# Kernel tuning notes

Measured on AMD Instinct MI355X. Metric: run time of the kernel, lower is better.

Reference implementation:

```python
import jax, jax.numpy as jnp
import numpy as np
from jax import lax

TOP_K = 6
NORM_MIN = 1e-12


def setup_inputs() -> dict:
    key = jax.random.key(0)
    k0, k1, k2, k3, k4, k5 = jax.random.split(key, 6)
    B, S, H, E, I = 2, 1024, 2048, 64, 512
    return {
        "hidden_states": jax.random.normal(k0, (B, S, H), dtype=jnp.float32),
        "gate_w": jax.random.normal(k1, (E, H), dtype=jnp.float32) * 0.02,
        "e_bias": jax.random.normal(k2, (E,), dtype=jnp.float32) * 0.01,
        "gate_proj": jax.random.normal(k3, (E, H, I), dtype=jnp.float32) * 0.02,
        "up_proj": jax.random.normal(k4, (E, H, I), dtype=jnp.float32) * 0.02,
        "down_proj": jax.random.normal(k5, (E, I, H), dtype=jnp.float32) * 0.02,
    }


def reference(hidden_states, gate_w, e_bias, gate_proj, up_proj, down_proj):
    B, S, H = hidden_states.shape
    E = gate_w.shape[0]
    x = hidden_states.reshape(-1, H)                      # [T, H]
    T = x.shape[0]

    # --- routing (done in float32 in the original) ---
    router_logits = x.astype(jnp.float32) @ gate_w.T      # [T, E]
    routing_probs = jax.nn.softmax(router_logits, axis=-1)
    # topk over bias-corrected scores, but weights come from raw probs
    _, selected = lax.top_k(routing_probs + e_bias[None, :], TOP_K)  # [T, k]
    w = jnp.take_along_axis(routing_probs, selected, axis=-1)        # [T, k]
    w = w / jnp.clip(w.sum(axis=-1, keepdims=True), NORM_MIN)
    w = w.astype(hidden_states.dtype)

    # combine weights: [T, E], zero for unselected experts
    combine = jnp.zeros((T, E), dtype=hidden_states.dtype)
    combine = combine.at[jnp.arange(T)[:, None], selected].add(w)

    # --- experts: SwiGLU MLP per expert, weighted-sum combine ---
    def step(acc, params):
        wg, wu, wd, c = params                            # wg,wu [H,I]; wd [I,H]; c [T]
        h = jax.nn.silu(x @ wg) * (x @ wu)                # [T, I]
        return acc + (h @ wd) * c[:, None], None

    init = jnp.zeros((T, H), dtype=hidden_states.dtype)
    final, _ = lax.scan(step, init, (gate_proj, up_proj, down_proj, combine.T))
    return final.reshape(-1), router_logits.reshape(-1)
```

## Files before the change

kernel.cpp:

```cpp
#include <hip/hip_runtime.h>
#include <math.h>

#define T_TOK 2048
#define H_DIM 2048
#define E_NUM 64
#define I_DIM 512
#define TOPK  6
#define NPAIR (T_TOK * TOPK)
#define MAXTILES 80

typedef __attribute__((ext_vector_type(8))) short s8;
typedef __attribute__((ext_vector_type(4))) float f4;
typedef __attribute__((ext_vector_type(8))) unsigned short u16x8;

static __device__ __forceinline__ unsigned short f2bf(float f) {
  unsigned int u = __float_as_uint(f);
  u += 0x7fff + ((u >> 16) & 1);
  return (unsigned short)(u >> 16);
}
static __device__ __forceinline__ unsigned int cvt_pk(float lo, float hi) {
  unsigned int r;
  asm("v_cvt_pk_bf16_f32 %0, %1, %2" : "=v"(r) : "v"(lo), "v"(hi));
  return r;
}
static __device__ __forceinline__ void gload_lds16(const void* g, void* l) {
  __builtin_amdgcn_global_load_lds(
      (const __attribute__((address_space(1))) unsigned int*)g,
      (__attribute__((address_space(3))) unsigned int*)l, 16, 0, 0);
}
#define SBAR()      __builtin_amdgcn_s_barrier()
#define SCHED0()    __builtin_amdgcn_sched_barrier(0)
#define WAIT_LGKM0() asm volatile("s_waitcnt lgkmcnt(0)" ::: "memory")
#define WAIT_VM0()   asm volatile("s_waitcnt vmcnt(0)" ::: "memory")
#define WAIT_VM2()   asm volatile("s_waitcnt vmcnt(2)" ::: "memory")
#define WAIT_VM4()   asm volatile("s_waitcnt vmcnt(4)" ::: "memory")

__global__ __launch_bounds__(512) void router_kernel(
    const float* __restrict__ x, const float* __restrict__ gw,
    const float* __restrict__ ebias, float* __restrict__ logits_out,
    int* __restrict__ sel, float* __restrict__ wsel)
{
  __shared__ float xs[4][H_DIM];
  __shared__ float lg[4][E_NUM];
  int t0 = blockIdx.x * 4;
  int tid = threadIdx.x;
  {
    float4* xsv = (float4*)&xs[0][0];
    const float4* src = (const float4*)(x + (size_t)t0 * H_DIM);
    for (int i = tid; i < 4 * H_DIM / 4; i += 512) xsv[i] = src[i];
  }
  __syncthreads();

  int wave = tid >> 6, lane = tid & 63;
  for (int ii = 0; ii < 4; ++ii) {
    int e0 = wave * 8 + ii * 2, e1 = e0 + 1;
    const float4* g0 = (const float4*)(gw + (size_t)e0 * H_DIM);
    const float4* g1 = (const float4*)(gw + (size_t)e1 * H_DIM);
    float s00=0.f,s01=0.f,s02=0.f,s03=0.f, s10=0.f,s11=0.f,s12=0.f,s13=0.f;
    for (int h4 = lane; h4 < H_DIM / 4; h4 += 64) {
      float4 w0 = g0[h4], w1 = g1[h4];
      float4 a0 = ((const float4*)xs[0])[h4];
      float4 a1 = ((const float4*)xs[1])[h4];
      float4 a2 = ((const float4*)xs[2])[h4];
      float4 a3 = ((const float4*)xs[3])[h4];
      s00 += w0.x*a0.x + w0.y*a0.y + w0.z*a0.z + w0.w*a0.w;
      s01 += w0.x*a1.x + w0.y*a1.y + w0.z*a1.z + w0.w*a1.w;
      s02 += w0.x*a2.x + w0.y*a2.y + w0.z*a2.z + w0.w*a2.w;
      s03 += w0.x*a3.x + w0.y*a3.y + w0.z*a3.z + w0.w*a3.w;
      s10 += w1.x*a0.x + w1.y*a0.y + w1.z*a0.z + w1.w*a0.w;
      s11 += w1.x*a1.x + w1.y*a1.y + w1.z*a1.z + w1.w*a1.w;
      s12 += w1.x*a2.x + w1.y*a2.y + w1.z*a2.z + w1.w*a2.w;
      s13 += w1.x*a3.x + w1.y*a3.y + w1.z*a3.z + w1.w*a3.w;
    }
    for (int off = 32; off; off >>= 1) {
      s00 += __shfl_down(s00, off); s01 += __shfl_down(s01, off);
      s02 += __shfl_down(s02, off); s03 += __shfl_down(s03, off);
      s10 += __shfl_down(s10, off); s11 += __shfl_down(s11, off);
      s12 += __shfl_down(s12, off); s13 += __shfl_down(s13, off);
    }
    if (lane == 0) {
      lg[0][e0]=s00; lg[1][e0]=s01; lg[2][e0]=s02; lg[3][e0]=s03;
      lg[0][e1]=s10; lg[1][e1]=s11; lg[2][e1]=s12; lg[3][e1]=s13;
    }
  }
  __syncthreads();

  if (tid < 256) {
    int tt = tid >> 6, e = tid & 63;
    logits_out[(size_t)(t0 + tt) * E_NUM + e] = lg[tt][e];
  }

  if (wave == 0) {
    for (int tt = 0; tt < 4; ++tt) {
      int t = t0 + tt;
      float v = lg[tt][lane];
      float m = v;
      for (int off = 32; off; off >>= 1) m = fmaxf(m, __shfl_xor(m, off));
      float ex = __expf(v - m);
      float sum = ex;
      for (int off = 32; off; off >>= 1) sum += __shfl_xor(sum, off);
      float prob = ex / sum;
      float sc = prob + ebias[lane];

      int selidx[TOPK]; float selw[TOPK]; float wsum = 0.f;
      #pragma unroll
      for (int k = 0; k < TOPK; ++k) {
        float mm = sc;
        for (int off = 32; off; off >>= 1) mm = fmaxf(mm, __shfl_xor(mm, off));
        unsigned long long ball = __ballot(sc == mm);
        int s = __ffsll(ball) - 1;
        float p = __shfl(prob, s);
        selidx[k] = s; selw[k] = p; wsum += p;
        if (lane == s) sc = -INFINITY;
      }
      if (lane == 0) {
        float inv = 1.f / fmaxf(wsum, 1e-12f);
        #pragma unroll
        for (int k = 0; k < TOPK; ++k) {
          sel[t * TOPK + k] = selidx[k];
          wsel[t * TOPK + k] = selw[k] * inv;
        }
      }
    }
  }
}

__global__ __launch_bounds__(64) void build_lists(
    const int* __restrict__ sel, const float* __restrict__ wsel,
    int* __restrict__ cnt, int* __restrict__ toklist, float* __restrict__ wtlist,
    int* __restrict__ posmap)
{
  int e = blockIdx.x, lane = threadIdx.x;
  int base = 0;
  for (int t0 = 0; t0 < T_TOK; t0 += 64) {
    int t = t0 + lane;
    int flag = 0, kk = 0; float w = 0.f;
    #pragma unroll
    for (int k = 0; k < TOPK; ++k)
      if (sel[t * TOPK + k] == e) { flag = 1; kk = k; w = wsel[t * TOPK + k]; }
    unsigned long long b = __ballot(flag);
    int pos = base + __popcll(b & ((1ull << lane) - 1ull));
    if (flag) {
      toklist[e * T_TOK + pos] = t;
      wtlist[e * T_TOK + pos] = w;
      posmap[t * TOPK + kk] = pos;
    }
    base += __popcll(b);
  }
  if (lane == 0) cnt[e] = base;
}

__global__ void scan_kernel(const int* __restrict__ cnt, int* __restrict__ texp,
                            int* __restrict__ tmap, int* __restrict__ ntile) {
  if (threadIdx.x == 0) {
    int nt = 0;
    for (int e = 0; e < E_NUM; ++e) {
      texp[e] = nt;
      int m = (cnt[e] + 255) >> 8;
      for (int tb = 0; tb < m && nt < MAXTILES; ++tb) tmap[nt++] = e * 16 + tb;
    }
    *ntile = nt;
  }
}

__global__ __launch_bounds__(256) void permute_kernel(
    const float* __restrict__ x, const int* __restrict__ cnt,
    const int* __restrict__ toklist, const int* __restrict__ tmap,
    const int* __restrict__ ntile, unsigned short* __restrict__ xt)
{
  int tile = blockIdx.y;
  if (tile >= *ntile) return;
  int ks = blockIdx.x;
  int em = tmap[tile], e = em >> 4, tb = em & 15;
  int n = cnt[e];
  int r = threadIdx.x;
  int tok = toklist[e * T_TOK + min(tb * 256 + r, n - 1)];
  const float4* src = (const float4*)(x + (size_t)tok * H_DIM + ks * 32);
  float4 v[8];
  #pragma unroll
  for (int q = 0; q < 8; ++q) v[q] = src[q];
  int g = (r >> 1) & 3;
  unsigned short* dst = xt + ((size_t)(tile * 64 + ks) * 1024 + r * 4) * 8;
  #pragma unroll
  for (int u = 0; u < 4; ++u) {
    int k16 = u ^ g;
    float4 a = v[2 * k16], b = v[2 * k16 + 1];
    u16x8 p;
    ((unsigned int*)&p)[0] = cvt_pk(a.x, a.y);
    ((unsigned int*)&p)[1] = cvt_pk(a.z, a.w);
    ((unsigned int*)&p)[2] = cvt_pk(b.x, b.y);
    ((unsigned int*)&p)[3] = cvt_pk(b.z, b.w);
    *(u16x8*)(dst + u * 8) = p;
  }
}

__global__ __launch_bounds__(512, 4) void gateup_kernel(
    const unsigned short* __restrict__ xt, const float* __restrict__ gp,
    const float* __restrict__ up, const int* __restrict__ tmap,
    const int* __restrict__ ntile, unsigned short* __restrict__ hat)
{
  __shared__ __align__(16) unsigned short A_lds[2][8192];
  __shared__ __align__(16) unsigned int   Bt[2][2][64 * 20];
  int tile = blockIdx.x;
  if (tile >= *ntile) return;
  int e = tmap[tile] >> 4;
  int ic = blockIdx.y, colbase = ic * 64;
  int tid = threadIdx.x, lane = tid & 63, wave = tid >> 6;
  int matc = wave >> 2, cw = wave & 3;
  int lrow = (lane >> 4) * 4, lcol = lane & 15, kgl = lane >> 4;
  int hp = tid & 15, cb = (tid >> 4) & 15, mstage = tid >> 8;
  const float* bsrc0 = ((mstage == 0) ? gp : up)
      + (size_t)e * (H_DIM * I_DIM) + colbase + (size_t)(2 * hp) * I_DIM + cb * 4;
  const unsigned short* achunk0 = xt + (size_t)tile * 64 * 1024 * 8;

  f4 acc[4][4];
  #pragma unroll
  for (int a = 0; a < 4; ++a)
    #pragma unroll
    for (int b = 0; b < 4; ++b) acc[a][b] = (f4)0.f;

  float4 p0, p1, q0, q1;
  {
    const unsigned short* s = achunk0 + (size_t)(wave * 128 + lane) * 8;
    gload_lds16(s,       &A_lds[0][(wave * 128) * 8]);
    gload_lds16(s + 512, &A_lds[0][(wave * 128 + 64) * 8]);
    p0 = *(const float4*)bsrc0;
    p1 = *(const float4*)(bsrc0 + I_DIM);
    WAIT_VM0();
    unsigned int* db = &Bt[0][mstage][cb * 4 * 20 + hp];
    db[0]  = cvt_pk(p0.x, p1.x); db[20] = cvt_pk(p0.y, p1.y);
    db[40] = cvt_pk(p0.z, p1.z); db[60] = cvt_pk(p0.w, p1.w);
    const float* b1 = bsrc0 + (size_t)32 * I_DIM;
    q0 = *(const float4*)b1;
    q1 = *(const float4*)(b1 + I_DIM);
    WAIT_LGKM0();
    SBAR();
    SCHED0();
  }

#define GU_STEP(K, C0, C1, N0, N1) do {                                            \
    if ((K) + 1 < 64) {                                                            \
      const unsigned short* s = achunk0 + ((size_t)((K) + 1) * 1024 + wave * 128 + lane) * 8; \
      gload_lds16(s,       &A_lds[((K) + 1) & 1][(wave * 128) * 8]);               \
      gload_lds16(s + 512, &A_lds[((K) + 1) & 1][(wave * 128 + 64) * 8]);          \
    }                                                                              \
    if ((K) + 2 < 64) {                                                            \
      const float* b = bsrc0 + (size_t)((K) + 2) * 32 * I_DIM;                     \
      N0 = *(const float4*)b; N1 = *(const float4*)(b + I_DIM);                    \
    }                                                                              \
    if ((K) + 2 < 64)      { WAIT_VM4(); }                                         \
    else if ((K) + 1 < 64) { WAIT_VM2(); }                                         \
    else                   { WAIT_VM0(); }                                         \
    if ((K) + 1 < 64) {                                                            \
      unsigned int* db = &Bt[((K) + 1) & 1][mstage][cb * 4 * 20 + hp];             \
      db[0]  = cvt_pk(C0.x, C1.x); db[20] = cvt_pk(C0.y, C1.y);                    \
      db[40] = cvt_pk(C0.z, C1.z); db[60] = cvt_pk(C0.w, C1.w);                    \
    }                                                                              \
    {                                                                              \
      s8 afr[4];                                                                   \
      _Pragma("unroll")                                                            \
      for (int mf = 0; mf < 4; ++mf) {                                             \
        int r = cw * 64 + mf * 16 + lcol;                                          \
        afr[mf] = *(s8*)&A_lds[(K) & 1][r * 32 + ((kgl ^ ((r >> 1) & 3)) * 8)];    \
      }                                                                            \
      _Pragma("unroll")                                                            \
      for (int nf = 0; nf < 4; ++nf) {                                             \
        s8 bfr = *(s8*)&Bt[(K) & 1][matc][(nf * 16 + lcol) * 20 + kgl * 4];        \
        _Pragma("unroll")                                                          \
        for (int mf = 0; mf < 4; ++mf)                                             \
          acc[mf][nf] = __builtin_amdgcn_mfma_f32_16x16x32_bf16(afr[mf], bfr, acc[mf][nf], 0, 0, 0); \
      }                                                                            \
    }                                                                              \
    if ((K) + 1 < 64) {                                                            \
      if ((K) + 2 < 64) { WAIT_VM2(); } else { WAIT_VM0(); }                       \
      WAIT_LGKM0(); SBAR(); SCHED0();                                              \
    }                                                                              \
  } while (0)

  for (int k = 0; k < 64; k += 2) {
    GU_STEP(k,     q0, q1, p0, p1);
    GU_STEP(k + 1, p0, p1, q0, q1);
  }
#undef GU_STEP

  f4* exch = (f4*)&Bt[0][0][0];
  unsigned short* hs = &A_lds[0][0];
  #pragma unroll
  for (int nf = 0; nf < 4; ++nf) {
    __syncthreads();
    if (wave >= 4) {
      #pragma unroll
      for (int mf = 0; mf < 4; ++mf)
        exch[((wave - 4) * 4 + mf) * 64 + lane] = acc[mf][nf];
    }
    __syncthreads();
    if (wave < 4) {
      #pragma unroll
      for (int mf = 0; mf < 4; ++mf) {
        f4 u = exch[(wave * 4 + mf) * 64 + lane];
        #pragma unroll
        for (int j = 0; j < 4; ++j) {
          float g = acc[mf][nf][j];
          float h = g / (1.f + __expf(-g)) * u[j];
          hs[(wave * 64 + mf * 16 + lrow + j) * 64 + nf * 16 + lcol] = f2bf(h);
        }
      }
    }
  }
  __syncthreads();
  #pragma unroll
  for (int c = 0; c < 2; ++c) {
    unsigned short* base = hat + (size_t)(tile * 16 + ic * 2 + c) * 1024 * 8;
    for (int uu = tid; uu < 1024; uu += 512) {
      int row = uu >> 2, k16 = (uu & 3) ^ ((row >> 1) & 3);
      *(u16x8*)(base + (size_t)uu * 8) = *(const u16x8*)&hs[row * 64 + c * 32 + k16 * 8];
    }
  }
}

__global__ __launch_bounds__(512, 4) void down_kernel(
    const unsigned short* __restrict__ hat, const float* __restrict__ dp,
    const int* __restrict__ cnt, const int* __restrict__ tmap,
    const int* __restrict__ ntile, const float* __restrict__ wtlist,
    unsigned short* __restrict__ pout)
{
  __shared__ __align__(16) unsigned short A_lds[2][8192];
  __shared__ __align__(16) unsigned int   Bt[2][2][64 * 20];
  __shared__ float swt[256];
  int tile = blockIdx.x;
  if (tile >= *ntile) return;
  int em = tmap[tile], e = em >> 4, tb = em & 15;
  int n = cnt[e];
  int hc = blockIdx.y, colbase = hc * 128;
  int tid = threadIdx.x, lane = tid & 63, wave = tid >> 6;
  int rg = wave & 3, cg = wave >> 2;
  int lrow = (lane >> 4) * 4, lcol = lane & 15, kgl = lane >> 4;
  int hp = tid & 15, cb = (tid >> 4) & 15, cgs = tid >> 8;
  const float* bsrc0 = dp + (size_t)e * (I_DIM * H_DIM) + colbase + cgs * 64
                       + (size_t)(2 * hp) * H_DIM + cb * 4;
  const unsigned short* achunk0 = hat + (size_t)tile * 16 * 1024 * 8;

  if (tid < 256) {
    int rr = tb * 256 + tid;
    swt[tid] = (rr < n) ? wtlist[e * T_TOK + rr] : 0.f;
  }

  f4 acc[4][4];
  #pragma unroll
  for (int a = 0; a < 4; ++a)
    #pragma unroll
    for (int b = 0; b < 4; ++b) acc[a][b] = (f4)0.f;

  float4 p0, p1, q0, q1;
  {
    const unsigned short* s = achunk0 + (size_t)(wave * 128 + lane) * 8;
    gload_lds16(s,       &A_lds[0][(wave * 128) * 8]);
    gload_lds16(s + 512, &A_lds[0][(wave * 128 + 64) * 8]);
    p0 = *(const float4*)bsrc0;
    p1 = *(const float4*)(bsrc0 + H_DIM);
    WAIT_VM0();
    unsigned int* db = &Bt[0][cgs][cb * 4 * 20 + hp];
    db[0]  = cvt_pk(p0.x, p1.x); db[20] = cvt_pk(p0.y, p1.y);
    db[40] = cvt_pk(p0.z, p1.z); db[60] = cvt_pk(p0.w, p1.w);
    const float* b1 = bsrc0 + (size_t)32 * H_DIM;
    q0 = *(const float4*)b1;
    q1 = *(const float4*)(b1 + H_DIM);
    WAIT_LGKM0();
    SBAR();
    SCHED0();
  }

#define DN_STEP(K, C0, C1, N0, N1) do {                                            \
    if ((K) + 1 < 16) {                                                            \
      const unsigned short* s = achunk0 + ((size_t)((K) + 1) * 1024 + wave * 128 + lane) * 8; \
      gload_lds16(s,       &A_lds[((K) + 1) & 1][(wave * 128) * 8]);               \
      gload_lds16(s + 512, &A_lds[((K) + 1) & 1][(wave * 128 + 64) * 8]);          \
    }                                                                              \
    if ((K) + 2 < 16) {                                                            \
      const float* b = bsrc0 + (size_t)((K) + 2) * 32 * H_DIM;                     \
      N0 = *(const float4*)b; N1 = *(const float4*)(b + H_DIM);                    \
    }                                                                              \
    if ((K) + 2 < 16)      { WAIT_VM4(); }                                         \
    else if ((K) + 1 < 16) { WAIT_VM2(); }                                         \
    else                   { WAIT_VM0(); }                                         \
    if ((K) + 1 < 16) {                                                            \
      unsigned int* db = &Bt[((K) + 1) & 1][cgs][cb * 4 * 20 + hp];                \
      db[0]  = cvt_pk(C0.x, C1.x); db[20] = cvt_pk(C0.y, C1.y);                    \
      db[40] = cvt_pk(C0.z, C1.z); db[60] = cvt_pk(C0.w, C1.w);                    \
    }                                                                              \
    {                                                                              \
      s8 afr[4];                                                                   \
      _Pragma("unroll")                                                            \
      for (int mf = 0; mf < 4; ++mf) {                                             \
        int r = rg * 64 + mf * 16 + lcol;                                          \
        afr[mf] = *(s8*)&A_lds[(K) & 1][r * 32 + ((kgl ^ ((r >> 1) & 3)) * 8)];    \
      }                                                                            \
      _Pragma("unroll")                                                            \
      for (int nf = 0; nf < 4; ++nf) {                                             \
        s8 bfr = *(s8*)&Bt[(K) & 1][cg][(nf * 16 + lcol) * 20 + kgl * 4];          \
        _Pragma("unroll")                                                          \
        for (int mf = 0; mf < 4; ++mf)                                             \
          acc[mf][nf] = __builtin_amdgcn_mfma_f32_16x16x32_bf16(afr[mf], bfr, acc[mf][nf], 0, 0, 0); \
      }                                                                            \
    }                                                                              \
    if ((K) + 1 < 16) {                                                            \
      if ((K) + 2 < 16) { WAIT_VM2(); } else { WAIT_VM0(); }                       \
      WAIT_LGKM0(); SBAR(); SCHED0();                                              \
    }                                                                              \
  } while (0)

  for (int k = 0; k < 16; k += 2) {
    DN_STEP(k,     q0, q1, p0, p1);
    DN_STEP(k + 1, p0, p1, q0, q1);
  }
#undef DN_STEP

  __syncthreads();
  unsigned short* hs = &A_lds[0][0];
  #pragma unroll
  for (int pass = 0; pass < 2; ++pass) {
    if (cg == pass) {
      #pragma unroll
      for (int mf = 0; mf < 4; ++mf)
        #pragma unroll
        for (int nf = 0; nf < 4; ++nf)
          #pragma unroll
          for (int j = 0; j < 4; ++j) {
            int r = rg * 64 + mf * 16 + lrow + j;
            hs[r * 64 + nf * 16 + lcol] = f2bf(acc[mf][nf][j] * swt[r]);
          }
    }
    __syncthreads();
    for (int u = tid; u < 2048; u += 512) {
      int row = u >> 3, unit = u & 7;
      *(u16x8*)(pout + (size_t)(tile * 256 + row) * H_DIM + colbase + pass * 64 + unit * 8) =
          *(const u16x8*)&hs[row * 64 + unit * 8];
    }
    __syncthreads();
  }
}

__global__ __launch_bounds__(256) void reduce_kernel(
    const unsigned short* __restrict__ pout, const int* __restrict__ sel,
    const int* __restrict__ posmap, const int* __restrict__ texp,
    float* __restrict__ out)
{
  int t = blockIdx.x, tid = threadIdx.x;
  int col = tid * 8;
  float acc[8];
  #pragma unroll
  for (int j = 0; j < 8; ++j) acc[j] = 0.f;
  #pragma unroll
  for (int k = 0; k < TOPK; ++k) {
    int e = sel[t * TOPK + k];
    int row = texp[e] * 256 + posmap[t * TOPK + k];
    u16x8 v = *(const u16x8*)(pout + (size_t)row * H_DIM + col);
    #pragma unroll
    for (int j = 0; j < 8; ++j)
      acc[j] += __uint_as_float((unsigned int)(unsigned short)v[j] << 16);
  }
  float4 o0 = {acc[0], acc[1], acc[2], acc[3]};
  float4 o1 = {acc[4], acc[5], acc[6], acc[7]};
  *(float4*)(out + (size_t)t * H_DIM + col)     = o0;
  *(float4*)(out + (size_t)t * H_DIM + col + 4) = o1;
}

extern "C" void kernel_launch(void* const* d_in, const int* in_sizes, int n_in,
                              void* d_out, int out_size, void* d_ws, size_t ws_size,
                              hipStream_t stream) {
  const float* hidden = (const float*)d_in[0];
  const float* gate_w = (const float*)d_in[1];
  const float* e_bias = (const float*)d_in[2];
  const float* gate_p = (const float*)d_in[3];
  const float* up_p   = (const float*)d_in[4];
  const float* down_p = (const float*)d_in[5];

  float* out_final  = (float*)d_out;
  float* out_logits = out_final + (size_t)T_TOK * H_DIM;

  int*   cnt     = (int*)d_ws;
  int*   texp    = cnt + 64;
  int*   ntile   = texp + 64;
  int*   tmap    = ntile + 16;
  int*   sel     = tmap + MAXTILES;
  float* wsel    = (float*)(sel + NPAIR);
  int*   posmap  = (int*)(wsel + NPAIR);
  int*   toklist = posmap + NPAIR;
  float* wtlist  = (float*)(toklist + E_NUM * T_TOK);
  unsigned short* xt  = (unsigned short*)(wtlist + E_NUM * T_TOK);
  unsigned short* hat = xt + (size_t)MAXTILES * 64 * 1024 * 8;
  unsigned short* pout = xt;

  router_kernel<<<T_TOK / 4, 512, 0, stream>>>(hidden, gate_w, e_bias, out_logits, sel, wsel);
  build_lists<<<E_NUM, 64, 0, stream>>>(sel, wsel, cnt, toklist, wtlist, posmap);
  scan_kernel<<<1, 64, 0, stream>>>(cnt, texp, tmap, ntile);
  permute_kernel<<<dim3(64, MAXTILES), 256, 0, stream>>>(hidden, cnt, toklist, tmap, ntile, xt);
  gateup_kernel<<<dim3(MAXTILES, I_DIM / 64), 512, 0, stream>>>(
      xt, gate_p, up_p, tmap, ntile, hat);
  down_kernel<<<dim3(MAXTILES, H_DIM / 128), 512, 0, stream>>>(
      hat, down_p, cnt, tmap, ntile, wtlist, pout);
  reduce_kernel<<<T_TOK, 256, 0, stream>>>(pout, sel, posmap, texp, out_final);
}
```

Baseline: 520.3 us.

## Load A fragments directly from global into registers instead of staging through LDS

The gate/up and down GEMM kernels no longer stage the bf16 activation tile in LDS via global_load_lds. Each wave now loads its own A fragments straight from global memory into double-buffered registers, which works because the permute and gate-up kernels now write activations in MFMA fragment order without the XOR swizzle. This removes LDS traffic and one barrier wait per k-step, but raises register pressure, so the occupancy hint drops from 4 to 2 blocks per CU. Waves that share rows also read the same A data redundantly from global/L2.

```diff
diff --git a/kernel.cpp b/kernel.cpp
--- a/kernel.cpp
+++ b/kernel.cpp
@@ -23,17 +23,12 @@
   asm("v_cvt_pk_bf16_f32 %0, %1, %2" : "=v"(r) : "v"(lo), "v"(hi));
   return r;
 }
-static __device__ __forceinline__ void gload_lds16(const void* g, void* l) {
-  __builtin_amdgcn_global_load_lds(
-      (const __attribute__((address_space(1))) unsigned int*)g,
-      (__attribute__((address_space(3))) unsigned int*)l, 16, 0, 0);
-}
 #define SBAR()      __builtin_amdgcn_s_barrier()
 #define SCHED0()    __builtin_amdgcn_sched_barrier(0)
 #define WAIT_LGKM0() asm volatile("s_waitcnt lgkmcnt(0)" ::: "memory")
 #define WAIT_VM0()   asm volatile("s_waitcnt vmcnt(0)" ::: "memory")
-#define WAIT_VM2()   asm volatile("s_waitcnt vmcnt(2)" ::: "memory")
 #define WAIT_VM4()   asm volatile("s_waitcnt vmcnt(4)" ::: "memory")
+#define WAIT_VM6()   asm volatile("s_waitcnt vmcnt(6)" ::: "memory")
 
 __global__ __launch_bounds__(512) void router_kernel(
     const float* __restrict__ x, const float* __restrict__ gw,
@@ -176,15 +171,10 @@
   int r = threadIdx.x;
   int tok = toklist[e * T_TOK + min(tb * 256 + r, n - 1)];
   const float4* src = (const float4*)(x + (size_t)tok * H_DIM + ks * 32);
-  float4 v[8];
-  #pragma unroll
-  for (int q = 0; q < 8; ++q) v[q] = src[q];
-  int g = (r >> 1) & 3;
   unsigned short* dst = xt + ((size_t)(tile * 64 + ks) * 1024 + r * 4) * 8;
   #pragma unroll
   for (int u = 0; u < 4; ++u) {
-    int k16 = u ^ g;
-    float4 a = v[2 * k16], b = v[2 * k16 + 1];
+    float4 a = src[2 * u], b = src[2 * u + 1];
     u16x8 p;
     ((unsigned int*)&p)[0] = cvt_pk(a.x, a.y);
     ((unsigned int*)&p)[1] = cvt_pk(a.z, a.w);
@@ -194,13 +184,13 @@
   }
 }
 
-__global__ __launch_bounds__(512, 4) void gateup_kernel(
+__global__ __launch_bounds__(512, 2) void gateup_kernel(
     const unsigned short* __restrict__ xt, const float* __restrict__ gp,
     const float* __restrict__ up, const int* __restrict__ tmap,
     const int* __restrict__ ntile, unsigned short* __restrict__ hat)
 {
-  __shared__ __align__(16) unsigned short A_lds[2][8192];
   __shared__ __align__(16) unsigned int   Bt[2][2][64 * 20];
+  __shared__ __align__(16) unsigned short hs[256 * 64];
   int tile = blockIdx.x;
   if (tile >= *ntile) return;
   int e = tmap[tile] >> 4;
@@ -212,6 +202,7 @@
   const float* bsrc0 = ((mstage == 0) ? gp : up)
       + (size_t)e * (H_DIM * I_DIM) + colbase + (size_t)(2 * hp) * I_DIM + cb * 4;
   const unsigned short* achunk0 = xt + (size_t)tile * 64 * 1024 * 8;
+  const unsigned short* abase = achunk0 + ((size_t)(cw * 64 + lcol) * 4 + kgl) * 8;
 
   f4 acc[4][4];
   #pragma unroll
@@ -219,17 +210,19 @@
     #pragma unroll
     for (int b = 0; b < 4; ++b) acc[a][b] = (f4)0.f;
 
+  s8 aA[4], aB[4];
   float4 p0, p1, q0, q1;
   {
-    const unsigned short* s = achunk0 + (size_t)(wave * 128 + lane) * 8;
-    gload_lds16(s,       &A_lds[0][(wave * 128) * 8]);
-    gload_lds16(s + 512, &A_lds[0][(wave * 128 + 64) * 8]);
     p0 = *(const float4*)bsrc0;
     p1 = *(const float4*)(bsrc0 + I_DIM);
     WAIT_VM0();
     unsigned int* db = &Bt[0][mstage][cb * 4 * 20 + hp];
     db[0]  = cvt_pk(p0.x, p1.x); db[20] = cvt_pk(p0.y, p1.y);
     db[40] = cvt_pk(p0.z, p1.z); db[60] = cvt_pk(p0.w, p1.w);
+    aA[0] = *(const s8*)(abase);
+    aA[1] = *(const s8*)(abase + 512);
+    aA[2] = *(const s8*)(abase + 1024);
+    aA[3] = *(const s8*)(abase + 1536);
     const float* b1 = bsrc0 + (size_t)32 * I_DIM;
     q0 = *(const float4*)b1;
     q1 = *(const float4*)(b1 + I_DIM);
@@ -238,53 +231,43 @@
     SCHED0();
   }
 
-#define GU_STEP(K, C0, C1, N0, N1) do {                                            \
+#define GU_STEP(K, BC0, BC1, BN0, BN1, AC, AN) do {                                \
     if ((K) + 1 < 64) {                                                            \
-      const unsigned short* s = achunk0 + ((size_t)((K) + 1) * 1024 + wave * 128 + lane) * 8; \
-      gload_lds16(s,       &A_lds[((K) + 1) & 1][(wave * 128) * 8]);               \
-      gload_lds16(s + 512, &A_lds[((K) + 1) & 1][(wave * 128 + 64) * 8]);          \
+      const unsigned short* s = abase + (size_t)((K) + 1) * 8192;                  \
+      AN[0] = *(const s8*)(s);                                                     \
+      AN[1] = *(const s8*)(s + 512);                                               \
+      AN[2] = *(const s8*)(s + 1024);                                              \
+      AN[3] = *(const s8*)(s + 1536);                                              \
     }                                                                              \
     if ((K) + 2 < 64) {                                                            \
       const float* b = bsrc0 + (size_t)((K) + 2) * 32 * I_DIM;                     \
-      N0 = *(const float4*)b; N1 = *(const float4*)(b + I_DIM);                    \
-    }                                                                              \
-    if ((K) + 2 < 64)      { WAIT_VM4(); }                                         \
-    else if ((K) + 1 < 64) { WAIT_VM2(); }                                         \
+      BN0 = *(const float4*)b; BN1 = *(const float4*)(b + I_DIM);                  \
+    }                                                                              \
+    if ((K) + 2 < 64)      { WAIT_VM6(); }                                         \
+    else if ((K) + 1 < 64) { WAIT_VM4(); }                                         \
     else                   { WAIT_VM0(); }                                         \
     if ((K) + 1 < 64) {                                                            \
       unsigned int* db = &Bt[((K) + 1) & 1][mstage][cb * 4 * 20 + hp];             \
-      db[0]  = cvt_pk(C0.x, C1.x); db[20] = cvt_pk(C0.y, C1.y);                    \
-      db[40] = cvt_pk(C0.z, C1.z); db[60] = cvt_pk(C0.w, C1.w);                    \
-    }                                                                              \
-    {                                                                              \
-      s8 afr[4];                                                                   \
+      db[0]  = cvt_pk(BC0.x, BC1.x); db[20] = cvt_pk(BC0.y, BC1.y);                \
+      db[40] = cvt_pk(BC0.z, BC1.z); db[60] = cvt_pk(BC0.w, BC1.w);                \
+    }                                                                              \
+    _Pragma("unroll")                                                              \
+    for (int nf = 0; nf < 4; ++nf) {                                               \
+      s8 bfr = *(s8*)&Bt[(K) & 1][matc][(nf * 16 + lcol) * 20 + kgl * 4];          \
       _Pragma("unroll")                                                            \
-      for (int mf = 0; mf < 4; ++mf) {                                             \
-        int r = cw * 64 + mf * 16 + lcol;                                          \
-        afr[mf] = *(s8*)&A_lds[(K) & 1][r * 32 + ((kgl ^ ((r >> 1) & 3)) * 8)];    \
-      }                                                                            \
-      _Pragma("unroll")                                                            \
-      for (int nf = 0; nf < 4; ++nf) {                                             \
-        s8 bfr = *(s8*)&Bt[(K) & 1][matc][(nf * 16 + lcol) * 20 + kgl * 4];        \
-        _Pragma("unroll")                                                          \
-        for (int mf = 0; mf < 4; ++mf)                                             \
-          acc[mf][nf] = __builtin_amdgcn_mfma_f32_16x16x32_bf16(afr[mf], bfr, acc[mf][nf], 0, 0, 0); \
-      }                                                                            \
-    }                                                                              \
-    if ((K) + 1 < 64) {                                                            \
-      if ((K) + 2 < 64) { WAIT_VM2(); } else { WAIT_VM0(); }                       \
-      WAIT_LGKM0(); SBAR(); SCHED0();                                              \
-    }                                                                              \
+      for (int mf = 0; mf < 4; ++mf)                                               \
+        acc[mf][nf] = __builtin_amdgcn_mfma_f32_16x16x32_bf16(AC[mf], bfr, acc[mf][nf], 0, 0, 0); \
+    }                                                                              \
+    if ((K) + 1 < 64) { WAIT_LGKM0(); SBAR(); SCHED0(); }                          \
   } while (0)
 
   for (int k = 0; k < 64; k += 2) {
-    GU_STEP(k,     q0, q1, p0, p1);
-    GU_STEP(k + 1, p0, p1, q0, q1);
+    GU_STEP(k,     q0, q1, p0, p1, aA, aB);
+    GU_STEP(k + 1, p0, p1, q0, q1, aB, aA);
   }
 #undef GU_STEP
 
   f4* exch = (f4*)&Bt[0][0][0];
-  unsigned short* hs = &A_lds[0][0];
   #pragma unroll
   for (int nf = 0; nf < 4; ++nf) {
     __syncthreads();
@@ -312,20 +295,20 @@
   for (int c = 0; c < 2; ++c) {
     unsigned short* base = hat + (size_t)(tile * 16 + ic * 2 + c) * 1024 * 8;
     for (int uu = tid; uu < 1024; uu += 512) {
-      int row = uu >> 2, k16 = (uu & 3) ^ ((row >> 1) & 3);
+      int row = uu >> 2, k16 = uu & 3;
       *(u16x8*)(base + (size_t)uu * 8) = *(const u16x8*)&hs[row * 64 + c * 32 + k16 * 8];
     }
   }
 }
 
-__global__ __launch_bounds__(512, 4) void down_kernel(
+__global__ __launch_bounds__(512, 2) void down_kernel(
     const unsigned short* __restrict__ hat, const float* __restrict__ dp,
     const int* __restrict__ cnt, const int* __restrict__ tmap,
     const int* __restrict__ ntile, const float* __restrict__ wtlist,
     unsigned short* __restrict__ pout)
 {
-  __shared__ __align__(16) unsigned short A_lds[2][8192];
   __shared__ __align__(16) unsigned int   Bt[2][2][64 * 20];
+  __shared__ __align__(16) unsigned short hs[256 * 64];
   __shared__ float swt[256];
   int tile = blockIdx.x;
   if (tile >= *ntile) return;
@@ -339,6 +322,7 @@
   const float* bsrc0 = dp + (size_t)e * (I_DIM * H_DIM) + colbase + cgs * 64
                        + (size_t)(2 * hp) * H_DIM + cb * 4;
   const unsigned short* achunk0 = hat + (size_t)tile * 16 * 1024 * 8;
+  const unsigned short* abase = achunk0 + ((size_t)(rg * 64 + lcol) * 4 + kgl) * 8;
 
   if (tid < 256) {
     int rr = tb * 256 + tid;
@@ -351,17 +335,19 @@
     #pragma unroll
     for (int b = 0; b < 4; ++b) acc[a][b] = (f4)0.f;
 
+  s8 aA[4], aB[4];
   float4 p0, p1, q0, q1;
   {
-    const unsigned short* s = achunk0 + (size_t)(wave * 128 + lane) * 8;
-    gload_lds16(s,       &A_lds[0][(wave * 128) * 8]);
-    gload_lds16(s + 512, &A_lds[0][(wave * 128 + 64) * 8]);
     p0 = *(const float4*)bsrc0;
     p1 = *(const float4*)(bsrc0 + H_DIM);
     WAIT_VM0();
     unsigned int* db = &Bt[0][cgs][cb * 4 * 20 + hp];
     db[0]  = cvt_pk(p0.x, p1.x); db[20] = cvt_pk(p0.y, p1.y);
     db[40] = cvt_pk(p0.z, p1.z); db[60] = cvt_pk(p0.w, p1.w);
+    aA[0] = *(const s8*)(abase);
+    aA[1] = *(const s8*)(abase + 512);
+    aA[2] = *(const s8*)(abase + 1024);
+    aA[3] = *(const s8*)(abase + 1536);
     const float* b1 = bsrc0 + (size_t)32 * H_DIM;
     q0 = *(const float4*)b1;
     q1 = *(const float4*)(b1 + H_DIM);
@@ -370,53 +356,43 @@
     SCHED0();
   }
 
-#define DN_STEP(K, C0, C1, N0, N1) do {                                            \
+#define DN_STEP(K, BC0, BC1, BN0, BN1, AC, AN) do {                                \
     if ((K) + 1 < 16) {                                                            \
-      const unsigned short* s = achunk0 + ((size_t)((K) + 1) * 1024 + wave * 128 + lane) * 8; \
-      gload_lds16(s,       &A_lds[((K) + 1) & 1][(wave * 128) * 8]);               \
-      gload_lds16(s + 512, &A_lds[((K) + 1) & 1][(wave * 128 + 64) * 8]);          \
+      const unsigned short* s = abase + (size_t)((K) + 1) * 8192;                  \
+      AN[0] = *(const s8*)(s);                                                     \
+      AN[1] = *(const s8*)(s + 512);                                               \
+      AN[2] = *(const s8*)(s + 1024);                                              \
+      AN[3] = *(const s8*)(s + 1536);                                              \
     }                                                                              \
     if ((K) + 2 < 16) {                                                            \
       const float* b = bsrc0 + (size_t)((K) + 2) * 32 * H_DIM;                     \
-      N0 = *(const float4*)b; N1 = *(const float4*)(b + H_DIM);                    \
-    }                                                                              \
-    if ((K) + 2 < 16)      { WAIT_VM4(); }                                         \
-    else if ((K) + 1 < 16) { WAIT_VM2(); }                                         \
+      BN0 = *(const float4*)b; BN1 = *(const float4*)(b + H_DIM);                  \
+    }                                                                              \
+    if ((K) + 2 < 16)      { WAIT_VM6(); }                                         \
+    else if ((K) + 1 < 16) { WAIT_VM4(); }                                         \
     else                   { WAIT_VM0(); }                                         \
     if ((K) + 1 < 16) {                                                            \
       unsigned int* db = &Bt[((K) + 1) & 1][cgs][cb * 4 * 20 + hp];                \
-      db[0]  = cvt_pk(C0.x, C1.x); db[20] = cvt_pk(C0.y, C1.y);                    \
-      db[40] = cvt_pk(C0.z, C1.z); db[60] = cvt_pk(C0.w, C1.w);                    \
-    }                                                                              \
-    {                                                                              \
-      s8 afr[4];                                                                   \
+      db[0]  = cvt_pk(BC0.x, BC1.x); db[20] = cvt_pk(BC0.y, BC1.y);                \
+      db[40] = cvt_pk(BC0.z, BC1.z); db[60] = cvt_pk(BC0.w, BC1.w);                \
+    }                                                                              \
+    _Pragma("unroll")                                                              \
+    for (int nf = 0; nf < 4; ++nf) {                                               \
+      s8 bfr = *(s8*)&Bt[(K) & 1][cg][(nf * 16 + lcol) * 20 + kgl * 4];            \
       _Pragma("unroll")                                                            \
-      for (int mf = 0; mf < 4; ++mf) {                                             \
-        int r = rg * 64 + mf * 16 + lcol;                                          \
-        afr[mf] = *(s8*)&A_lds[(K) & 1][r * 32 + ((kgl ^ ((r >> 1) & 3)) * 8)];    \
-      }                                                                            \
-      _Pragma("unroll")                                                            \
-      for (int nf = 0; nf < 4; ++nf) {                                             \
-        s8 bfr = *(s8*)&Bt[(K) & 1][cg][(nf * 16 + lcol) * 20 + kgl * 4];          \
-        _Pragma("unroll")                                                          \
-        for (int mf = 0; mf < 4; ++mf)                                             \
-          acc[mf][nf] = __builtin_amdgcn_mfma_f32_16x16x32_bf16(afr[mf], bfr, acc[mf][nf], 0, 0, 0); \
-      }                                                                            \
-    }                                                                              \
-    if ((K) + 1 < 16) {                                                            \
-      if ((K) + 2 < 16) { WAIT_VM2(); } else { WAIT_VM0(); }                       \
-      WAIT_LGKM0(); SBAR(); SCHED0();                                              \
-    }                                                                              \
+      for (int mf = 0; mf < 4; ++mf)                                               \
+        acc[mf][nf] = __builtin_amdgcn_mfma_f32_16x16x32_bf16(AC[mf], bfr, acc[mf][nf], 0, 0, 0); \
+    }                                                                              \
+    if ((K) + 1 < 16) { WAIT_LGKM0(); SBAR(); SCHED0(); }                          \
   } while (0)
 
   for (int k = 0; k < 16; k += 2) {
-    DN_STEP(k,     q0, q1, p0, p1);
-    DN_STEP(k + 1, p0, p1, q0, q1);
+    DN_STEP(k,     q0, q1, p0, p1, aA, aB);
+    DN_STEP(k + 1, p0, p1, q0, q1, aB, aA);
   }
 #undef DN_STEP
 
   __syncthreads();
-  unsigned short* hs = &A_lds[0][0];
   #pragma unroll
   for (int pass = 0; pass < 2; ++pass) {
     if (cg == pass) {
```

New measurement: 545.4 us. +4.8%, slower.
